# Optimization experiments

Hardware: AMD Instinct MI355X
Metric: run time of the kernel (lower is better)

The kernel has to match this reference:

```python
import jax, jax.numpy as jnp
import numpy as np

N_NODES = 10000
N_EDGES = 160000
NEG_SLOPE = 0.2
DIMS = [(128, 1024), (1024, 512), (512, 128)]
NUM_CLASSES = 64


def _glorot(k, shape):
    lim = np.sqrt(6.0 / (shape[0] + shape[1])).astype(np.float32)
    return jax.random.uniform(k, shape, jnp.float32, -lim, lim)


def setup_inputs() -> dict:
    key = jax.random.key(0)
    ks = iter(jax.random.split(key, 32))
    inp = {
        'x': jax.random.normal(next(ks), (N_NODES, DIMS[0][0]), jnp.float32),
        'edge_index': jax.random.randint(next(ks), (2, N_EDGES), 0, N_NODES, jnp.int64),
    }
    for i, (fin, fout) in enumerate(DIMS, start=1):
        inp[f'Wl{i}'] = _glorot(next(ks), (fin, fout))
        inp[f'bl{i}'] = jnp.zeros((fout,), jnp.float32)
        inp[f'Wr{i}'] = _glorot(next(ks), (fin, fout))
        inp[f'br{i}'] = jnp.zeros((fout,), jnp.float32)
        inp[f'att{i}'] = _glorot(next(ks), (1, fout))[0]
        inp[f'b{i}'] = jnp.zeros((fout,), jnp.float32)
    inp['Wc'] = _glorot(next(ks), (DIMS[-1][1], NUM_CLASSES))
    inp['bc'] = jnp.zeros((NUM_CLASSES,), jnp.float32)
    return inp


def _gatv2(x, src, dst, Wl, bl, Wr, br, att, b):
    # PyG GATv2Conv, heads=1, add_self_loops=True (self-loops appended by caller)
    n = x.shape[0]
    xl = x @ Wl + bl          # source-side transform [N, F]
    xr = x @ Wr + br          # target-side transform [N, F]
    m = xl[src] + xr[dst]     # [E, F] per-edge message
    e = jax.nn.leaky_relu(m, NEG_SLOPE) @ att  # [E] attention logits
    # segment softmax over incoming edges of each dst node
    emax = jax.ops.segment_max(e, dst, num_segments=n)
    ez = jnp.exp(e - emax[dst])
    denom = jax.ops.segment_sum(ez, dst, num_segments=n)
    alpha = ez / denom[dst]
    out = jax.ops.segment_sum(alpha[:, None] * xl[src], dst, num_segments=n)
    return out + b


def reference(x, edge_index, Wl1, bl1, Wr1, br1, att1, b1,
              Wl2, bl2, Wr2, br2, att2, b2,
              Wl3, bl3, Wr3, br3, att3, b3, Wc, bc):
    n = x.shape[0]
    loops = jnp.arange(n, dtype=edge_index.dtype)
    src = jnp.concatenate([edge_index[0], loops])
    dst = jnp.concatenate([edge_index[1], loops])
    h = jax.nn.relu(_gatv2(x, src, dst, Wl1, bl1, Wr1, br1, att1, b1))
    h = jax.nn.relu(_gatv2(h, src, dst, Wl2, bl2, Wr2, br2, att2, b2))
    h = jax.nn.relu(_gatv2(h, src, dst, Wl3, bl3, Wr3, br3, att3, b3))
    return h @ Wc + bc
```

## Files before the change

### kernel.cpp

```cpp
#include <hip/hip_runtime.h>


typedef __attribute__((ext_vector_type(8))) short bf16x8;
typedef __attribute__((ext_vector_type(4))) float f32x4;

__device__ __forceinline__ unsigned short bf16rn(float x) {
    union { float f; unsigned int u; } v; v.f = x;
    unsigned int r = v.u + 0x7FFF + ((v.u >> 16) & 1);
    return (unsigned short)(r >> 16);
}
__device__ __forceinline__ float bf16tof(unsigned short h) {
    union { unsigned int u; float f; } v; v.u = ((unsigned int)h) << 16;
    return v.f;
}

typedef __attribute__((address_space(1))) const void* gptr_t;
typedef __attribute__((address_space(3))) void* sptr_t;
__device__ __forceinline__ void gload_lds16(const void* g, void* l) {
    __builtin_amdgcn_global_load_lds((gptr_t)g, (sptr_t)l, 16, 0, 0);
}


__global__ __launch_bounds__(256) void splitT_kernel(
    const float* __restrict__ W, unsigned short* __restrict__ Th,
    unsigned short* __restrict__ Tl, int K, int F)
{
    __shared__ float tile[32][33];
    const int tx = threadIdx.x & 31, ty = threadIdx.x >> 5;
    const int k0 = blockIdx.x * 32, f0 = blockIdx.y * 32;
#pragma unroll
    for (int i = 0; i < 32; i += 8)
        tile[ty + i][tx] = W[(size_t)(k0 + ty + i) * F + f0 + tx];
    __syncthreads();
#pragma unroll
    for (int i = 0; i < 32; i += 8) {
        int f = f0 + ty + i, k = k0 + tx;
        float v = tile[tx][ty + i];
        unsigned short h = bf16rn(v);
        Th[(size_t)f * K + k] = h;
        Tl[(size_t)f * K + k] = bf16rn(v - bf16tof(h));
    }
}

__global__ void split_kernel(const float* __restrict__ X,
                             unsigned short* __restrict__ Hi,
                             unsigned short* __restrict__ Lo, int n4)
{
    int i = blockIdx.x * blockDim.x + threadIdx.x;
    if (i >= n4) return;
    float4 v = ((const float4*)X)[i];
    ushort4 h, l;
    h.x = bf16rn(v.x); l.x = bf16rn(v.x - bf16tof(h.x));
    h.y = bf16rn(v.y); l.y = bf16rn(v.y - bf16tof(h.y));
    h.z = bf16rn(v.z); l.z = bf16rn(v.z - bf16tof(h.z));
    h.w = bf16rn(v.w); l.w = bf16rn(v.w - bf16tof(h.w));
    ((ushort4*)Hi)[i] = h;
    ((ushort4*)Lo)[i] = l;
}


template<int BM, int BN>
__global__ __launch_bounds__(256) void gemm_mfma_t(
    const unsigned short* __restrict__ Ahi, const unsigned short* __restrict__ Alo,
    int M, int K,
    const unsigned short* __restrict__ WThA, const unsigned short* __restrict__ WTlA,
    const unsigned short* __restrict__ WThB, const unsigned short* __restrict__ WTlB,
    const float* __restrict__ biasA, const float* __restrict__ biasB,
    float* __restrict__ CA, float* __restrict__ CB, int F, int nby)
{
    constexpr int GA = BM / 16, GB = BN / 16;
    constexpr int NJ = (2 * GA + 2 * GB) / 4;
    constexpr int WM = BM / 2, WN = BN / 2;
    constexpr int MI = WM / 16, NI = WN / 16;
    constexpr int ASZ = BM * 32, BSZ = BN * 32;

    __shared__ unsigned short Ash[2 * ASZ];
    __shared__ unsigned short Asl[2 * ASZ];
    __shared__ unsigned short Bsh[2 * BSZ];
    __shared__ unsigned short Bsl[2 * BSZ];

    const int t = threadIdx.x;
    const int lane = t & 63, wave = t >> 6;

    const int nwg = (int)gridDim.x;
    const int bid = (int)blockIdx.x;
    const int q = nwg >> 3, r = nwg & 7;
    const int xcd = bid & 7, slot = bid >> 3;
    const int gidx = (xcd < r) ? (xcd * (q + 1) + slot)
                               : (r * (q + 1) + (xcd - r) * q + slot);
    const int bx = gidx / nby, byi = gidx % nby;

    const int nyh = nby >> 1;
    const int half = (byi >= nyh) ? 1 : 0;
    const int colBase = (byi - half * nyh) * BN;
    const unsigned short* WTh = half ? WThB : WThA;
    const unsigned short* WTl = half ? WTlB : WTlA;
    const float* bias = half ? biasB : biasA;
    float* C = half ? CB : CA;
    const int rowBase = bx * BM;

    const int wr = wave >> 1, wc = wave & 1;
    const int fr = lane & 15, g = lane >> 4;

    const int srow = lane >> 2;
    const int schunk = ((lane & 3) ^ ((lane >> 3) & 3)) * 8;

    const unsigned short* gsrc[NJ];
    unsigned short* ldst[NJ];
#pragma unroll
    for (int j = 0; j < NJ; ++j) {
        const int grp = wave + 4 * j;
        if (grp < GA) {
            int ga = rowBase + grp * 16 + srow; if (ga > M - 1) ga = M - 1;
            gsrc[j] = Ahi + (size_t)ga * K + schunk;
            ldst[j] = &Ash[grp * 512];
        } else if (grp < 2 * GA) {
            const int r16 = grp - GA;
            int ga = rowBase + r16 * 16 + srow; if (ga > M - 1) ga = M - 1;
            gsrc[j] = Alo + (size_t)ga * K + schunk;
            ldst[j] = &Asl[r16 * 512];
        } else if (grp < 2 * GA + GB) {
            const int r16 = grp - 2 * GA;
            const int gb = colBase + r16 * 16 + srow;
            gsrc[j] = WTh + (size_t)gb * K + schunk;
            ldst[j] = &Bsh[r16 * 512];
        } else {
            const int r16 = grp - 2 * GA - GB;
            const int gb = colBase + r16 * 16 + srow;
            gsrc[j] = WTl + (size_t)gb * K + schunk;
            ldst[j] = &Bsl[r16 * 512];
        }
    }

    auto stage = [&](int dbuf, int koff) {
#pragma unroll
        for (int j = 0; j < NJ; ++j) {
            const int grp = wave + 4 * j;
            const int pl = (grp < 2 * GA) ? ASZ : BSZ;
            gload_lds16(gsrc[j] + koff, ldst[j] + dbuf * pl);
        }
    };

    f32x4 acc[MI][NI];
#pragma unroll
    for (int i = 0; i < MI; ++i)
#pragma unroll
        for (int j = 0; j < NI; ++j) acc[i][j] = (f32x4)(0.f);

    const int fragoff = (fr * 4 + (g ^ ((fr >> 1) & 3))) * 8;

    stage(0, 0);
    __syncthreads();

    const int nt = K >> 5;
    for (int tt = 0; tt < nt; ++tt) {
        const int cur = tt & 1;
        if (tt + 1 < nt) stage(cur ^ 1, (tt + 1) * 32);

        bf16x8 ah[MI], al[MI], bh[NI], bl[NI];
#pragma unroll
        for (int mi = 0; mi < MI; ++mi) {
            ah[mi] = *(const bf16x8*)&Ash[cur * ASZ + (wr * MI + mi) * 512 + fragoff];
            al[mi] = *(const bf16x8*)&Asl[cur * ASZ + (wr * MI + mi) * 512 + fragoff];
        }
#pragma unroll
        for (int ni = 0; ni < NI; ++ni) {
            bh[ni] = *(const bf16x8*)&Bsh[cur * BSZ + (wc * NI + ni) * 512 + fragoff];
            bl[ni] = *(const bf16x8*)&Bsl[cur * BSZ + (wc * NI + ni) * 512 + fragoff];
        }
#pragma unroll
        for (int mi = 0; mi < MI; ++mi)
#pragma unroll
            for (int ni = 0; ni < NI; ++ni) {
                acc[mi][ni] = __builtin_amdgcn_mfma_f32_16x16x32_bf16(ah[mi], bh[ni], acc[mi][ni], 0, 0, 0);
                acc[mi][ni] = __builtin_amdgcn_mfma_f32_16x16x32_bf16(ah[mi], bl[ni], acc[mi][ni], 0, 0, 0);
                acc[mi][ni] = __builtin_amdgcn_mfma_f32_16x16x32_bf16(al[mi], bh[ni], acc[mi][ni], 0, 0, 0);
            }
        __syncthreads();
    }

#pragma unroll
    for (int mi = 0; mi < MI; ++mi) {
        const int row0 = rowBase + wr * WM + mi * 16 + g * 4;
#pragma unroll
        for (int ni = 0; ni < NI; ++ni) {
            const int col = colBase + wc * WN + ni * 16 + fr;
            const float b = bias[col];
#pragma unroll
            for (int rr = 0; rr < 4; ++rr) {
                const int row = row0 + rr;
                if (row < M) C[(size_t)row * F + col] = acc[mi][ni][rr] + b;
            }
        }
    }
}


static constexpr int BMc = 64, BNc = 64, BKc = 16;

__global__ __launch_bounds__(256) void gemm_bias_kernel(
    const float* __restrict__ A, const float* __restrict__ W,
    const float* __restrict__ bias, float* __restrict__ C,
    int M, int K, int F)
{
    __shared__ float As[BKc][BMc];
    __shared__ float Bs[BKc][BNc];
    const int t = threadIdx.x;
    const int bm = blockIdx.x, bn = blockIdx.y;
    const int ty = t >> 4, tx = t & 15;
    const int rowBase = bm * BMc;
    const int colBase = bn * BNc;
    const int aRow = t & 63;
    const int aK = (t >> 6) << 2;
    const int gARow = min(rowBase + aRow, M - 1);
    const int bRow = t >> 4;
    const int bCol = (t & 15) << 2;

    float acc[4][4] = {{0.f, 0.f, 0.f, 0.f}};

    for (int k0 = 0; k0 < K; k0 += BKc) {
        float4 av = *(const float4*)&A[(size_t)gARow * K + k0 + aK];
        float4 bv = *(const float4*)&W[(size_t)(k0 + bRow) * F + colBase + bCol];
        As[aK + 0][aRow] = av.x;
        As[aK + 1][aRow] = av.y;
        As[aK + 2][aRow] = av.z;
        As[aK + 3][aRow] = av.w;
        *(float4*)&Bs[bRow][bCol] = bv;
        __syncthreads();
#pragma unroll
        for (int kk = 0; kk < BKc; ++kk) {
            float4 a4 = *(const float4*)&As[kk][ty << 2];
            float4 b4 = *(const float4*)&Bs[kk][tx << 2];
            float ar[4] = {a4.x, a4.y, a4.z, a4.w};
            float br_[4] = {b4.x, b4.y, b4.z, b4.w};
#pragma unroll
            for (int i = 0; i < 4; ++i)
#pragma unroll
                for (int j = 0; j < 4; ++j)
                    acc[i][j] += ar[i] * br_[j];
        }
        __syncthreads();
    }

    float4 bias4 = *(const float4*)&bias[colBase + (tx << 2)];
    float bb[4] = {bias4.x, bias4.y, bias4.z, bias4.w};
#pragma unroll
    for (int i = 0; i < 4; ++i) {
        int r = rowBase + (ty << 2) + i;
        if (r < M) {
            float4 o;
            o.x = acc[i][0] + bb[0];
            o.y = acc[i][1] + bb[1];
            o.z = acc[i][2] + bb[2];
            o.w = acc[i][3] + bb[3];
            *(float4*)&C[(size_t)r * F + colBase + (tx << 2)] = o;
        }
    }
}


__global__ void zero_ints_kernel(int* __restrict__ p, int n)
{
    int i = blockIdx.x * blockDim.x + threadIdx.x;
    if (i < n) p[i] = 0;
}

__device__ inline void edge_src_dst(const int* __restrict__ ei, int edge,
                                    int E_orig, int& src, int& dst)
{
    if (edge < E_orig) {
        src = ei[edge];
        dst = ei[E_orig + edge];
    } else {
        src = dst = edge - E_orig;
    }
}

__global__ void count_kernel(const int* __restrict__ ei, int E_orig, int E_tot,
                             int* __restrict__ counts)
{
    int e = blockIdx.x * blockDim.x + threadIdx.x;
    if (e >= E_tot) return;
    int src, dst;
    edge_src_dst(ei, e, E_orig, src, dst);
    atomicAdd(&counts[dst], 1);
}

__global__ __launch_bounds__(256) void scan_kernel(const int* __restrict__ counts, int n,
                                                   int* __restrict__ offsets,
                                                   int* __restrict__ cursor)
{
    __shared__ int part[256];
    const int t = threadIdx.x;
    const int chunk = (n + 255) >> 8;
    const int begin = t * chunk;
    const int end = min(begin + chunk, n);
    int s = 0;
    for (int i = begin; i < end; ++i) s += counts[i];
    part[t] = s;
    __syncthreads();
    for (int off = 1; off < 256; off <<= 1) {
        int v = (t >= off) ? part[t - off] : 0;
        __syncthreads();
        part[t] += v;
        __syncthreads();
    }
    int run = (t == 0) ? 0 : part[t - 1];
    for (int i = begin; i < end; ++i) {
        offsets[i] = run;
        cursor[i] = run;
        run += counts[i];
    }
    if (t == 255) offsets[n] = part[255];
}

__global__ void fill_kernel(const int* __restrict__ ei, int E_orig, int E_tot,
                            int* __restrict__ cursor, int* __restrict__ csr_src)
{
    int e = blockIdx.x * blockDim.x + threadIdx.x;
    if (e >= E_tot) return;
    int src, dst;
    edge_src_dst(ei, e, E_orig, src, dst);
    int pos = atomicAdd(&cursor[dst], 1);
    csr_src[pos] = src;
}


template<int F, bool SPLIT, int B>
__global__ __launch_bounds__(256) void fused_gat_wave_kernel(
    const float* __restrict__ xl, const float* __restrict__ xr,
    const float* __restrict__ att, const int* __restrict__ offsets,
    const int* __restrict__ csr_src, const float* __restrict__ bias,
    float* __restrict__ out_f32,
    unsigned short* __restrict__ out_hi, unsigned short* __restrict__ out_lo,
    int N)
{
    constexpr int VEC = F / 64;
    constexpr int CW = (VEC >= 4) ? 4 : VEC;
    constexpr int NC = VEC / CW;
    const int wave = threadIdx.x >> 6, lane = threadIdx.x & 63;
    const int n = blockIdx.x * 4 + wave;
    if (n >= N) return;
    const int start = offsets[n], end = offsets[n + 1];

    float xr_r[VEC], att_r[VEC], acc[VEC];
#pragma unroll
    for (int j = 0; j < NC; ++j)
#pragma unroll
        for (int c = 0; c < CW; ++c) {
            const int f = j * 64 * CW + lane * CW + c;
            xr_r[j * CW + c] = xr[(size_t)n * F + f];
            att_r[j * CW + c] = att[f];
            acc[j * CW + c] = 0.f;
        }

    float m = -1e30f, d = 0.f;

    for (int i = start; i < end; i += B) {
        int srcs[B];
#pragma unroll
        for (int b = 0; b < B; ++b) srcs[b] = csr_src[min(i + b, end - 1)];

        float r[B][VEC];
#pragma unroll
        for (int b = 0; b < B; ++b) {
            const float* row = xl + (size_t)srcs[b] * F;
#pragma unroll
            for (int j = 0; j < NC; ++j) {
                if constexpr (CW == 4) {
                    float4 v = *(const float4*)&row[j * 256 + lane * 4];
                    r[b][j * 4 + 0] = v.x; r[b][j * 4 + 1] = v.y;
                    r[b][j * 4 + 2] = v.z; r[b][j * 4 + 3] = v.w;
                } else {
                    float2 v = *(const float2*)&row[lane * 2];
                    r[b][0] = v.x; r[b][1] = v.y;
                }
            }
        }

        float p[B];
#pragma unroll
        for (int b = 0; b < B; ++b) {
            float pp = 0.f;
#pragma unroll
            for (int v = 0; v < VEC; ++v) {
                float mm = r[b][v] + xr_r[v];
                mm = fmaxf(mm, 0.2f * mm);
                pp += mm * att_r[v];
            }
            p[b] = pp;
        }

#pragma unroll
        for (int off = 32; off; off >>= 1)
#pragma unroll
            for (int b = 0; b < B; ++b) p[b] += __shfl_xor(p[b], off);

#pragma unroll
        for (int b = 0; b < B; ++b)
            if (i + b >= end) p[b] = -1e30f;

        float bmax = p[0];
#pragma unroll
        for (int b = 1; b < B; ++b) bmax = fmaxf(bmax, p[b]);
        const float nm = fmaxf(m, bmax);
        const float scale = __expf(m - nm);
        float w[B], wsum = 0.f;
#pragma unroll
        for (int b = 0; b < B; ++b) { w[b] = __expf(p[b] - nm); wsum += w[b]; }
        d = d * scale + wsum;
#pragma unroll
        for (int v = 0; v < VEC; ++v) {
            float a = acc[v] * scale;
#pragma unroll
            for (int b = 0; b < B; ++b) a += w[b] * r[b][v];
            acc[v] = a;
        }
        m = nm;
    }

    const float inv = 1.0f / d;
#pragma unroll
    for (int j = 0; j < NC; ++j) {
        float o[CW];
#pragma unroll
        for (int c = 0; c < CW; ++c) {
            const int f = j * 64 * CW + lane * CW + c;
            o[c] = fmaxf(acc[j * CW + c] * inv + bias[f], 0.f);
        }
        const size_t base = (size_t)n * F + j * 64 * CW + lane * CW;
        if constexpr (SPLIT) {
            if constexpr (CW == 4) {
                ushort4 h, l;
                h.x = bf16rn(o[0]); l.x = bf16rn(o[0] - bf16tof(h.x));
                h.y = bf16rn(o[1]); l.y = bf16rn(o[1] - bf16tof(h.y));
                h.z = bf16rn(o[2]); l.z = bf16rn(o[2] - bf16tof(h.z));
                h.w = bf16rn(o[3]); l.w = bf16rn(o[3] - bf16tof(h.w));
                *(ushort4*)&out_hi[base] = h;
                *(ushort4*)&out_lo[base] = l;
            } else {
                ushort2 h, l;
                h.x = bf16rn(o[0]); l.x = bf16rn(o[0] - bf16tof(h.x));
                h.y = bf16rn(o[1]); l.y = bf16rn(o[1] - bf16tof(h.y));
                *(ushort2*)&out_hi[base] = h;
                *(ushort2*)&out_lo[base] = l;
            }
        } else {
            if constexpr (CW == 4) {
                float4 v = {o[0], o[1], o[2], o[3]};
                *(float4*)&out_f32[base] = v;
            } else {
                float2 v = {o[0], o[1]};
                *(float2*)&out_f32[base] = v;
            }
        }
    }
}


extern "C" void kernel_launch(void* const* d_in, const int* in_sizes, int n_in,
                              void* d_out, int out_size, void* d_ws, size_t ws_size,
                              hipStream_t stream)
{
    const float* x   = (const float*)d_in[0];
    const int*   ei  = (const int*)d_in[1];
    const float* Wl1 = (const float*)d_in[2];
    const float* bl1 = (const float*)d_in[3];
    const float* Wr1 = (const float*)d_in[4];
    const float* br1 = (const float*)d_in[5];
    const float* at1 = (const float*)d_in[6];
    const float* b1  = (const float*)d_in[7];
    const float* Wl2 = (const float*)d_in[8];
    const float* bl2 = (const float*)d_in[9];
    const float* Wr2 = (const float*)d_in[10];
    const float* br2 = (const float*)d_in[11];
    const float* at2 = (const float*)d_in[12];
    const float* b2  = (const float*)d_in[13];
    const float* Wl3 = (const float*)d_in[14];
    const float* bl3 = (const float*)d_in[15];
    const float* Wr3 = (const float*)d_in[16];
    const float* br3 = (const float*)d_in[17];
    const float* at3 = (const float*)d_in[18];
    const float* b3  = (const float*)d_in[19];
    const float* Wc  = (const float*)d_in[20];
    const float* bc  = (const float*)d_in[21];

    const int N = in_sizes[0] / 128;
    const int E_orig = in_sizes[1] / 2;
    const int E_tot = E_orig + N;

    size_t off = 0;
    auto alloc = [&](size_t bytes) -> char* {
        char* p = (char*)d_ws + off;
        off += (bytes + 255) & ~(size_t)255;
        return p;
    };
    float* bufA = (float*)alloc((size_t)N * 1024 * 4);
    float* bufB = (float*)alloc((size_t)N * 1024 * 4);
    unsigned short* S_hi = (unsigned short*)alloc((size_t)N * 1024 * 2);
    unsigned short* S_lo = (unsigned short*)alloc((size_t)N * 1024 * 2);
    unsigned short* WThl = (unsigned short*)alloc((size_t)524288 * 2);
    unsigned short* WTll = (unsigned short*)alloc((size_t)524288 * 2);
    unsigned short* WThr = (unsigned short*)alloc((size_t)524288 * 2);
    unsigned short* WTlr = (unsigned short*)alloc((size_t)524288 * 2);
    int* counts  = (int*)alloc((size_t)N * 4);
    int* offsets = (int*)alloc((size_t)(N + 1) * 4);
    int* cursor  = (int*)alloc((size_t)N * 4);
    int* csr_src = (int*)alloc((size_t)E_tot * 4);
    (void)ws_size; (void)n_in; (void)out_size;

    const int eb = (E_tot + 255) / 256;
    const int mb128 = (N + 127) / 128;
    const int mb64  = (N + 63) / 64;
    const int nb4 = (N + 3) / 4;

    zero_ints_kernel<<<(N + 255) / 256, 256, 0, stream>>>(counts, N);
    count_kernel<<<eb, 256, 0, stream>>>(ei, E_orig, E_tot, counts);
    scan_kernel<<<1, 256, 0, stream>>>(counts, N, offsets, cursor);
    fill_kernel<<<eb, 256, 0, stream>>>(ei, E_orig, E_tot, cursor, csr_src);

    split_kernel<<<(N * 128 / 4 + 255) / 256, 256, 0, stream>>>(x, S_hi, S_lo, N * 128 / 4);

    splitT_kernel<<<dim3(128 / 32, 1024 / 32), 256, 0, stream>>>(Wl1, WThl, WTll, 128, 1024);
    splitT_kernel<<<dim3(128 / 32, 1024 / 32), 256, 0, stream>>>(Wr1, WThr, WTlr, 128, 1024);
    gemm_mfma_t<128, 128><<<mb128 * 16, 256, 0, stream>>>(
        S_hi, S_lo, N, 128, WThl, WTll, WThr, WTlr, bl1, br1, bufA, bufB, 1024, 16);
    fused_gat_wave_kernel<1024, true, 4><<<nb4, 256, 0, stream>>>(
        bufA, bufB, at1, offsets, csr_src, b1, nullptr, S_hi, S_lo, N);

    splitT_kernel<<<dim3(1024 / 32, 512 / 32), 256, 0, stream>>>(Wl2, WThl, WTll, 1024, 512);
    splitT_kernel<<<dim3(1024 / 32, 512 / 32), 256, 0, stream>>>(Wr2, WThr, WTlr, 1024, 512);
    gemm_mfma_t<128, 128><<<mb128 * 8, 256, 0, stream>>>(
        S_hi, S_lo, N, 1024, WThl, WTll, WThr, WTlr, bl2, br2, bufA, bufB, 512, 8);
    fused_gat_wave_kernel<512, true, 4><<<nb4, 256, 0, stream>>>(
        bufA, bufB, at2, offsets, csr_src, b2, nullptr, S_hi, S_lo, N);

    splitT_kernel<<<dim3(512 / 32, 128 / 32), 256, 0, stream>>>(Wl3, WThl, WTll, 512, 128);
    splitT_kernel<<<dim3(512 / 32, 128 / 32), 256, 0, stream>>>(Wr3, WThr, WTlr, 512, 128);
    gemm_mfma_t<64, 64><<<mb64 * 4, 256, 0, stream>>>(
        S_hi, S_lo, N, 512, WThl, WTll, WThr, WTlr, bl3, br3, bufA, bufB, 128, 4);
    fused_gat_wave_kernel<128, false, 8><<<nb4, 256, 0, stream>>>(
        bufA, bufB, at3, offsets, csr_src, b3, bufB, nullptr, nullptr, N);

    gemm_bias_kernel<<<dim3((N + BMc - 1) / BMc, 64 / BNc), 256, 0, stream>>>(
        bufB, Wc, bc, (float*)d_out, N, 128, 64);
}
```

Baseline: 395.8 us.

## Split each node's feature dimension across two waves for layers one and two

Adds a GAT aggregation kernel that puts two wavefronts on each destination node, each handling half of the feature dimension. The partial attention logits are combined through shared memory with a block barrier on every edge batch. Each lane holds half as many feature values, which lowers register pressure for F=1024 and F=512 and should allow more resident waves to hide gather latency. The cost is one extra __syncthreads per batch and a launch of one block per node. The older single-wave kernel has only its local variables renamed.

```diff
diff --git a/kernel.cpp b/kernel.cpp
--- a/kernel.cpp
+++ b/kernel.cpp
@@ -327,6 +327,132 @@
 
 
 template<int F, bool SPLIT, int B>
+__global__ __launch_bounds__(128) void fused_gat_2wave_kernel(
+    const float* __restrict__ xl, const float* __restrict__ xr,
+    const float* __restrict__ att, const int* __restrict__ offsets,
+    const int* __restrict__ csr_src, const float* __restrict__ bias,
+    float* __restrict__ out_f32,
+    unsigned short* __restrict__ out_hi, unsigned short* __restrict__ out_lo,
+    int N)
+{
+    constexpr int VEC = F / 128;
+    constexpr int NC = VEC / 4;
+    const int w = threadIdx.x >> 6, lane = threadIdx.x & 63;
+    const int n = blockIdx.x;
+    if (n >= N) return;
+    const int start = offsets[n], end = offsets[n + 1];
+    const int baseF = w * (F / 2);
+
+    __shared__ float wsum[2][2][B];
+
+    float xr_r[VEC], att_r[VEC], acc[VEC];
+#pragma unroll
+    for (int j = 0; j < NC; ++j)
+#pragma unroll
+        for (int c = 0; c < 4; ++c) {
+            const int f = baseF + j * 256 + lane * 4 + c;
+            xr_r[j * 4 + c] = xr[(size_t)n * F + f];
+            att_r[j * 4 + c] = att[f];
+            acc[j * 4 + c] = 0.f;
+        }
+
+    float m = -1e30f, d = 0.f;
+    int par = 0;
+
+    for (int i = start; i < end; i += B, par ^= 1) {
+        int srcs[B];
+#pragma unroll
+        for (int b = 0; b < B; ++b) srcs[b] = csr_src[min(i + b, end - 1)];
+
+        float r[B][VEC];
+#pragma unroll
+        for (int b = 0; b < B; ++b) {
+            const float* row = xl + (size_t)srcs[b] * F + baseF;
+#pragma unroll
+            for (int j = 0; j < NC; ++j) {
+                float4 v = *(const float4*)&row[j * 256 + lane * 4];
+                r[b][j * 4 + 0] = v.x; r[b][j * 4 + 1] = v.y;
+                r[b][j * 4 + 2] = v.z; r[b][j * 4 + 3] = v.w;
+            }
+        }
+
+        float p[B];
+#pragma unroll
+        for (int b = 0; b < B; ++b) {
+            float pp = 0.f;
+#pragma unroll
+            for (int v = 0; v < VEC; ++v) {
+                float mm = r[b][v] + xr_r[v];
+                mm = fmaxf(mm, 0.2f * mm);
+                pp += mm * att_r[v];
+            }
+            p[b] = pp;
+        }
+
+#pragma unroll
+        for (int off = 32; off; off >>= 1)
+#pragma unroll
+            for (int b = 0; b < B; ++b) p[b] += __shfl_xor(p[b], off);
+
+        if (lane == 0) {
+#pragma unroll
+            for (int b = 0; b < B; ++b) wsum[par][w][b] = p[b];
+        }
+        __syncthreads();
+
+        float e[B];
+#pragma unroll
+        for (int b = 0; b < B; ++b) {
+            e[b] = p[b] + wsum[par][1 - w][b];
+            if (i + b >= end) e[b] = -1e30f;
+        }
+
+        float bmax = e[0];
+#pragma unroll
+        for (int b = 1; b < B; ++b) bmax = fmaxf(bmax, e[b]);
+        const float nm = fmaxf(m, bmax);
+        const float scale = __expf(m - nm);
+        float wg[B], wsumv = 0.f;
+#pragma unroll
+        for (int b = 0; b < B; ++b) { wg[b] = __expf(e[b] - nm); wsumv += wg[b]; }
+        d = d * scale + wsumv;
+#pragma unroll
+        for (int v = 0; v < VEC; ++v) {
+            float a = acc[v] * scale;
+#pragma unroll
+            for (int b = 0; b < B; ++b) a += wg[b] * r[b][v];
+            acc[v] = a;
+        }
+        m = nm;
+    }
+
+    const float inv = 1.0f / d;
+#pragma unroll
+    for (int j = 0; j < NC; ++j) {
+        float o[4];
+#pragma unroll
+        for (int c = 0; c < 4; ++c) {
+            const int f = baseF + j * 256 + lane * 4 + c;
+            o[c] = fmaxf(acc[j * 4 + c] * inv + bias[f], 0.f);
+        }
+        const size_t base = (size_t)n * F + baseF + j * 256 + lane * 4;
+        if constexpr (SPLIT) {
+            ushort4 h, l;
+            h.x = bf16rn(o[0]); l.x = bf16rn(o[0] - bf16tof(h.x));
+            h.y = bf16rn(o[1]); l.y = bf16rn(o[1] - bf16tof(h.y));
+            h.z = bf16rn(o[2]); l.z = bf16rn(o[2] - bf16tof(h.z));
+            h.w = bf16rn(o[3]); l.w = bf16rn(o[3] - bf16tof(h.w));
+            *(ushort4*)&out_hi[base] = h;
+            *(ushort4*)&out_lo[base] = l;
+        } else {
+            float4 v = {o[0], o[1], o[2], o[3]};
+            *(float4*)&out_f32[base] = v;
+        }
+    }
+}
+
+
+template<int F, bool SPLIT, int B>
 __global__ __launch_bounds__(256) void fused_gat_wave_kernel(
     const float* __restrict__ xl, const float* __restrict__ xr,
     const float* __restrict__ att, const int* __restrict__ offsets,
@@ -405,15 +531,15 @@
         for (int b = 1; b < B; ++b) bmax = fmaxf(bmax, p[b]);
         const float nm = fmaxf(m, bmax);
         const float scale = __expf(m - nm);
-        float w[B], wsum = 0.f;
-#pragma unroll
-        for (int b = 0; b < B; ++b) { w[b] = __expf(p[b] - nm); wsum += w[b]; }
-        d = d * scale + wsum;
+        float wg[B], wsumv = 0.f;
+#pragma unroll
+        for (int b = 0; b < B; ++b) { wg[b] = __expf(p[b] - nm); wsumv += wg[b]; }
+        d = d * scale + wsumv;
 #pragma unroll
         for (int v = 0; v < VEC; ++v) {
             float a = acc[v] * scale;
 #pragma unroll
-            for (int b = 0; b < B; ++b) a += w[b] * r[b][v];
+            for (int b = 0; b < B; ++b) a += wg[b] * r[b][v];
             acc[v] = a;
         }
         m = nm;
@@ -525,14 +651,14 @@
     splitT_kernel<<<dim3(128 / 32, 1024 / 32), 256, 0, stream>>>(Wr1, WThr, WTlr, 128, 1024);
     gemm_mfma_t<128, 128><<<mb128 * 16, 256, 0, stream>>>(
         S_hi, S_lo, N, 128, WThl, WTll, WThr, WTlr, bl1, br1, bufA, bufB, 1024, 16);
-    fused_gat_wave_kernel<1024, true, 4><<<nb4, 256, 0, stream>>>(
+    fused_gat_2wave_kernel<1024, true, 4><<<N, 128, 0, stream>>>(
         bufA, bufB, at1, offsets, csr_src, b1, nullptr, S_hi, S_lo, N);
 
     splitT_kernel<<<dim3(1024 / 32, 512 / 32), 256, 0, stream>>>(Wl2, WThl, WTll, 1024, 512);
     splitT_kernel<<<dim3(1024 / 32, 512 / 32), 256, 0, stream>>>(Wr2, WThr, WTlr, 1024, 512);
     gemm_mfma_t<128, 128><<<mb128 * 8, 256, 0, stream>>>(
         S_hi, S_lo, N, 1024, WThl, WTll, WThr, WTlr, bl2, br2, bufA, bufB, 512, 8);
-    fused_gat_wave_kernel<512, true, 4><<<nb4, 256, 0, stream>>>(
+    fused_gat_2wave_kernel<512, true, 4><<<N, 128, 0, stream>>>(
         bufA, bufB, at2, offsets, csr_src, b2, nullptr, S_hi, S_lo, N);
 
     splitT_kernel<<<dim3(512 / 32, 128 / 32), 256, 0, stream>>>(Wl3, WThl, WTll, 512, 128);
```

New measurement: 400.7 us. Within noise of the previous version (+1.2%).

## Split GAT attention into feature-sliced logits, edge softmax, and sliced aggregation kernels

Applied to the files above, without the earlier changes.

Replaces the fused per-node online-softmax GAT kernel for layers 1 and 2 with three passes. The first computes partial attention logits per 64-feature slice, the second reduces them and runs the segment softmax per node, and the third aggregates weighted source rows per slice. Launches are split across feature slices so each pass touches a smaller working set of the xl/xr rows, which is meant to improve cache locality of the random gathers. The cost is that xl rows are gathered twice, and partial logits and alpha go through global memory with extra launches.

```diff
diff --git a/kernel.cpp b/kernel.cpp
--- a/kernel.cpp
+++ b/kernel.cpp
@@ -326,6 +326,120 @@
 }
 
 
+template<int F, int NS, int NSL>
+__global__ __launch_bounds__(256) void slice_logits_kernel(
+    const float* __restrict__ xl, const float* __restrict__ xr,
+    const float* __restrict__ att, const int* __restrict__ offsets,
+    const int* __restrict__ csr_src, float* __restrict__ e_part,
+    int N, int s_base)
+{
+    const int wave = threadIdx.x >> 6, lane = threadIdx.x & 63;
+    const int s = s_base + (int)blockIdx.x % NSL;
+    const int n = ((int)blockIdx.x / NSL) * 4 + wave;
+    if (n >= N) return;
+    const int start = offsets[n], end = offsets[n + 1];
+    const int g = lane >> 3, j = lane & 7;
+    const int f0 = s * 64 + j;
+
+    float xr_r[8], att_r[8];
+#pragma unroll
+    for (int k = 0; k < 8; ++k) {
+        xr_r[k] = __builtin_nontemporal_load(&xr[(size_t)n * F + f0 + 8 * k]);
+        att_r[k] = att[f0 + 8 * k];
+    }
+
+    for (int i = start; i < end; i += 8) {
+        const int src = csr_src[min(i + g, end - 1)];
+        const float* row = xl + (size_t)src * F + f0;
+        float a = 0.f;
+#pragma unroll
+        for (int k = 0; k < 8; ++k) {
+            float mm = row[8 * k] + xr_r[k];
+            mm = fmaxf(mm, 0.2f * mm);
+            a += mm * att_r[k];
+        }
+        a += __shfl_xor(a, 1);
+        a += __shfl_xor(a, 2);
+        a += __shfl_xor(a, 4);
+        if (j == 0 && i + g < end)
+            __builtin_nontemporal_store(a, &e_part[(size_t)(i + g) * NS + s]);
+    }
+}
+
+
+template<int NS>
+__global__ __launch_bounds__(256) void edge_softmax_kernel(
+    const float* __restrict__ e_part, const int* __restrict__ offsets,
+    float* __restrict__ alpha, float* __restrict__ invd, int N)
+{
+    const int wave = threadIdx.x >> 6, lane = threadIdx.x & 63;
+    const int n = blockIdx.x * 4 + wave;
+    if (n >= N) return;
+    const int start = offsets[n], end = offsets[n + 1];
+
+    float m = -1e30f;
+    for (int i = start + lane; i < end; i += 64) {
+        float e = 0.f;
+#pragma unroll
+        for (int sIdx = 0; sIdx < NS; ++sIdx) e += e_part[(size_t)i * NS + sIdx];
+        alpha[i] = e;
+        m = fmaxf(m, e);
+    }
+#pragma unroll
+    for (int off = 32; off; off >>= 1) m = fmaxf(m, __shfl_xor(m, off));
+    float d = 0.f;
+    for (int i = start + lane; i < end; i += 64) {
+        float w = __expf(alpha[i] - m);
+        alpha[i] = w;
+        d += w;
+    }
+#pragma unroll
+    for (int off = 32; off; off >>= 1) d += __shfl_xor(d, off);
+    if (lane == 0) invd[n] = 1.0f / d;
+}
+
+
+template<int F, int NS, int NSL, bool SPLIT>
+__global__ __launch_bounds__(256) void slice_agg_kernel(
+    const float* __restrict__ xl, const float* __restrict__ alpha,
+    const float* __restrict__ invd, const int* __restrict__ offsets,
+    const int* __restrict__ csr_src, const float* __restrict__ bias,
+    float* __restrict__ out_f32, unsigned short* __restrict__ out_hi,
+    unsigned short* __restrict__ out_lo, int N, int s_base)
+{
+    const int wave = threadIdx.x >> 6, lane = threadIdx.x & 63;
+    const int s = s_base + (int)blockIdx.x % NSL;
+    const int n = ((int)blockIdx.x / NSL) * 4 + wave;
+    if (n >= N) return;
+    const int start = offsets[n], end = offsets[n + 1];
+    const int f0 = s * 64 + lane;
+
+    float acc = 0.f;
+    for (int i = start; i < end; i += 8) {
+        int srcs[8]; float w[8];
+#pragma unroll
+        for (int b = 0; b < 8; ++b) {
+            const int idx = min(i + b, end - 1);
+            srcs[b] = csr_src[idx];
+            w[b] = (i + b < end) ? alpha[i + b] : 0.f;
+        }
+#pragma unroll
+        for (int b = 0; b < 8; ++b)
+            acc += w[b] * xl[(size_t)srcs[b] * F + f0];
+    }
+
+    const float o = fmaxf(acc * invd[n] + bias[f0], 0.f);
+    const size_t oidx = (size_t)n * F + f0;
+    if constexpr (SPLIT) {
+        const unsigned short h = bf16rn(o);
+        __builtin_nontemporal_store(h, &out_hi[oidx]);
+        __builtin_nontemporal_store(bf16rn(o - bf16tof(h)), &out_lo[oidx]);
+    } else {
+        __builtin_nontemporal_store(o, &out_f32[oidx]);
+    }
+}
+
+
 template<int F, bool SPLIT, int B>
 __global__ __launch_bounds__(256) void fused_gat_wave_kernel(
     const float* __restrict__ xl, const float* __restrict__ xr,
@@ -405,15 +519,15 @@
         for (int b = 1; b < B; ++b) bmax = fmaxf(bmax, p[b]);
         const float nm = fmaxf(m, bmax);
         const float scale = __expf(m - nm);
-        float w[B], wsum = 0.f;
-#pragma unroll
-        for (int b = 0; b < B; ++b) { w[b] = __expf(p[b] - nm); wsum += w[b]; }
-        d = d * scale + wsum;
+        float wg[B], wsumv = 0.f;
+#pragma unroll
+        for (int b = 0; b < B; ++b) { wg[b] = __expf(p[b] - nm); wsumv += wg[b]; }
+        d = d * scale + wsumv;
 #pragma unroll
         for (int v = 0; v < VEC; ++v) {
             float a = acc[v] * scale;
 #pragma unroll
-            for (int b = 0; b < B; ++b) a += w[b] * r[b][v];
+            for (int b = 0; b < B; ++b) a += wg[b] * r[b][v];
             acc[v] = a;
         }
         m = nm;
@@ -503,6 +617,9 @@
     unsigned short* WTll = (unsigned short*)alloc((size_t)524288 * 2);
     unsigned short* WThr = (unsigned short*)alloc((size_t)524288 * 2);
     unsigned short* WTlr = (unsigned short*)alloc((size_t)524288 * 2);
+    float* e_part = (float*)alloc((size_t)E_tot * 16 * 4);
+    float* alpha  = (float*)alloc((size_t)E_tot * 4);
+    float* invd   = (float*)alloc((size_t)N * 4);
     int* counts  = (int*)alloc((size_t)N * 4);
     int* offsets = (int*)alloc((size_t)(N + 1) * 4);
     int* cursor  = (int*)alloc((size_t)N * 4);
@@ -525,15 +642,25 @@
     splitT_kernel<<<dim3(128 / 32, 1024 / 32), 256, 0, stream>>>(Wr1, WThr, WTlr, 128, 1024);
     gemm_mfma_t<128, 128><<<mb128 * 16, 256, 0, stream>>>(
         S_hi, S_lo, N, 128, WThl, WTll, WThr, WTlr, bl1, br1, bufA, bufB, 1024, 16);
-    fused_gat_wave_kernel<1024, true, 4><<<nb4, 256, 0, stream>>>(
-        bufA, bufB, at1, offsets, csr_src, b1, nullptr, S_hi, S_lo, N);
+    slice_logits_kernel<1024, 16, 8><<<nb4 * 8, 256, 0, stream>>>(
+        bufA, bufB, at1, offsets, csr_src, e_part, N, 0);
+    slice_logits_kernel<1024, 16, 8><<<nb4 * 8, 256, 0, stream>>>(
+        bufA, bufB, at1, offsets, csr_src, e_part, N, 8);
+    edge_softmax_kernel<16><<<nb4, 256, 0, stream>>>(e_part, offsets, alpha, invd, N);
+    slice_agg_kernel<1024, 16, 8, true><<<nb4 * 8, 256, 0, stream>>>(
+        bufA, alpha, invd, offsets, csr_src, b1, nullptr, S_hi, S_lo, N, 0);
+    slice_agg_kernel<1024, 16, 8, true><<<nb4 * 8, 256, 0, stream>>>(
+        bufA, alpha, invd, offsets, csr_src, b1, nullptr, S_hi, S_lo, N, 8);
 
     splitT_kernel<<<dim3(1024 / 32, 512 / 32), 256, 0, stream>>>(Wl2, WThl, WTll, 1024, 512);
     splitT_kernel<<<dim3(1024 / 32, 512 / 32), 256, 0, stream>>>(Wr2, WThr, WTlr, 1024, 512);
     gemm_mfma_t<128, 128><<<mb128 * 8, 256, 0, stream>>>(
         S_hi, S_lo, N, 1024, WThl, WTll, WThr, WTlr, bl2, br2, bufA, bufB, 512, 8);
-    fused_gat_wave_kernel<512, true, 4><<<nb4, 256, 0, stream>>>(
-        bufA, bufB, at2, offsets, csr_src, b2, nullptr, S_hi, S_lo, N);
+    slice_logits_kernel<512, 8, 8><<<nb4 * 8, 256, 0, stream>>>(
+        bufA, bufB, at2, offsets, csr_src, e_part, N, 0);
+    edge_softmax_kernel<8><<<nb4, 256, 0, stream>>>(e_part, offsets, alpha, invd, N);
+    slice_agg_kernel<512, 8, 8, true><<<nb4 * 8, 256, 0, stream>>>(
+        bufA, alpha, invd, offsets, csr_src, b2, nullptr, S_hi, S_lo, N, 0);
 
     splitT_kernel<<<dim3(512 / 32, 128 / 32), 256, 0, stream>>>(Wl3, WThl, WTll, 512, 128);
     splitT_kernel<<<dim3(512 / 32, 128 / 32), 256, 0, stream>>>(Wr3, WThr, WTlr, 512, 128);
```

Result: slower. 544.5 us (+37.6%).
